# Kernel tuning notes

Hardware: AMD Instinct MI355X
Metric: run time of the kernel (lower is better)

The kernel has to match this reference:

```python
import jax, jax.numpy as jnp
import numpy as np

ALPHA = 4.0  # spikingjelly default Sigmoid surrogate alpha
BN_EPS = 1e-5

@jax.custom_vjp
def _spike(v):
    return (v >= 0.0).astype(v.dtype)

def _spike_fwd(v):
    return _spike(v), v

def _spike_bwd(v, g):
    s = jax.nn.sigmoid(ALPHA * v)
    return (g * ALPHA * s * (1.0 - s),)

_spike.defvjp(_spike_fwd, _spike_bwd)

def lif(x, v_th):
    # Single-step LIFNode(tau=2, v_reset=0) starting from v=0:
    # v = v + (x - v)/tau = x/2 ; spike = Heaviside(v - v_th)
    return _spike(x * 0.5 - v_th)

def bn(x, p):
    # p: [4, C] = gamma, beta, running_mean, running_var (inference BN)
    g, b, m, v = p
    scale = g * jax.lax.rsqrt(v + BN_EPS)
    return x * scale[None, :, None, None] + (b - m * scale)[None, :, None, None]

def conv1x1(x, w):
    # x: [B,C,H,W], w: [O,C]
    return jnp.einsum('bchw,oc->bohw', x, w)

def dwconv3x3(x, w):
    # depthwise 3x3, w: [C,3,3]
    C = x.shape[1]
    return jax.lax.conv_general_dilated(
        x, w[:, None], (1, 1), 'SAME',
        feature_group_count=C,
        dimension_numbers=('NCHW', 'OIHW', 'NCHW'))

def branch(x, w1, dw, w2, bns):
    # RepConv: conv1x1 -> BN -> (dw3x3 -> pw1x1 -> BN), then the extra Sequential BN
    x = bn(conv1x1(x, w1), bns[0])
    x = bn(conv1x1(dwconv3x3(x, dw), w2), bns[1])
    return bn(x, bns[2])

def setup_inputs() -> dict:
    key = jax.random.key(0)
    ks = jax.random.split(key, 5)
    B, C, H, W = 16, 256, 80, 80
    x = jax.random.normal(ks[0], (B, C, H, W), jnp.float32) * 2.0  # so LIFs actually fire
    w1 = jax.random.normal(ks[1], (4, C, C), jnp.float32) * 0.06
    dw = jax.random.normal(ks[2], (4, C, 3, 3), jnp.float32) * 0.3
    w2 = jax.random.normal(ks[3], (4, C, C), jnp.float32) * 0.06
    bn_params = jax.random.uniform(ks[4], (4, 3, 4, C), jnp.float32, 0.1, 1.0)
    return {"x": x, "w1": w1, "dw": dw, "w2": w2, "bn_params": bn_params}

def reference(x, w1, dw, w2, bn_params):
    scale = 0.125
    xs = lif(x, 1.0)                                   # head_lif
    q = branch(xs, w1[0], dw[0], w2[0], bn_params[0])  # q_conv (q_lif unused in source)
    k = branch(xs, w1[1], dw[1], w2[1], bn_params[1])  # k_conv (k_lif unused in source)
    v = branch(xs, w1[2], dw[2], w2[2], bn_params[2])  # v_conv
    v = lif(v, 1.0)                                    # v_lif -> binary spikes
    # k.transpose(-2,-1) @ v : per (b,c) [W,H] @ [H,W] -> [W,W]
    kv = jnp.einsum('bchw,bchu->bcwu', k, v)
    # q @ kv : [H,W] @ [W,W] -> [H,W]
    attn = jnp.einsum('bchw,bcwu->bchu', q, kv) * scale
    s = lif(attn, 0.5)                                 # attn_lif, v_threshold=0.5
    return branch(s, w1[3], dw[3], w2[3], bn_params[3])  # proj_conv
```

## Files before the change

### kernel.cpp

```cpp
#include <hip/hip_runtime.h>
#include <hip/hip_bf16.h>
#include <cstdint>
#include <cstddef>
#include <cmath>

typedef unsigned short u16;
typedef unsigned char  u8;
typedef unsigned int   u32;
typedef __attribute__((ext_vector_type(8))) short short8;
typedef __attribute__((ext_vector_type(4))) float f32x4;
typedef __attribute__((ext_vector_type(4))) u16 u16x4;

#define CCH 256
#define HWP 6400

__device__ __forceinline__ u16 f2bf(float f) {
  u32 u = __float_as_uint(f);
  u = (u + 0x7FFFu + ((u >> 16) & 1u)) >> 16;
  return (u16)u;
}
__device__ __forceinline__ float bf2f(u16 h) { return __uint_as_float(((u32)h) << 16); }
__device__ __forceinline__ void split3(float v, u16& h, u16& m, u16& l) {
  h = f2bf(v); float r = v - bf2f(h);
  m = f2bf(r); l = f2bf(r - bf2f(m));
}
__device__ __forceinline__ void gl_lds16(const void* g, void* l) {
  __builtin_amdgcn_global_load_lds((const __attribute__((address_space(1))) unsigned int*)g,
                                   (__attribute__((address_space(3))) unsigned int*)l,
                                   16, 0, 0);
}

__global__ __launch_bounds__(256) void fold_weights(
    const float* __restrict__ w1, const float* __restrict__ w2,
    const float* __restrict__ bnp,
    u16* __restrict__ w1h, u16* __restrict__ w1m, u16* __restrict__ w1l,
    u16* __restrict__ w2h, u16* __restrict__ w2m, u16* __restrict__ w2l,
    float* __restrict__ b0f, float* __restrict__ b2f)
{
  int i = blockIdx.x >> 8, o = blockIdx.x & 255, c = threadIdx.x;
  const float* bp = bnp + i * 3072;
  double g0 = bp[0 + o],    be0 = bp[256 + o],  m0 = bp[512 + o],  v0 = bp[768 + o];
  double g1 = bp[1024 + o], be1 = bp[1280 + o], m1 = bp[1536 + o], v1 = bp[1792 + o];
  double g2 = bp[2048 + o], be2 = bp[2304 + o], m2 = bp[2560 + o], v2 = bp[2816 + o];
  double s0 = g0 / sqrt(v0 + 1e-5);
  double s1 = g1 / sqrt(v1 + 1e-5);
  double s2 = g2 / sqrt(v2 + 1e-5);
  size_t ro = (size_t)(i * 256 + o) * 256;
  float wa = (float)(s0 * (double)w1[ro + c]);
  float wb = (float)(s1 * s2 * (double)w2[ro + c]);
  u16 h, m, l;
  split3(wa, h, m, l); w1h[ro + c] = h; w1m[ro + c] = m; w1l[ro + c] = l;
  split3(wb, h, m, l); w2h[ro + c] = h; w2m[ro + c] = m; w2l[ro + c] = l;
  if (c == 0) {
    b0f[i * 256 + o] = (float)(be0 - m0 * s0);
    b2f[i * 256 + o] = (float)(s2 * (be1 - m1 * s1) + be2 - m2 * s2);
  }
}

__global__ __launch_bounds__(256) void head_spike(
    const float* __restrict__ x, u8* __restrict__ xs, int b0)
{
  __shared__ u8 tile[64][68];
  int z = blockIdx.z, c0 = blockIdx.y << 6, p0 = blockIdx.x << 6;
  int tid = threadIdx.x;
  const float* xb = x + ((size_t)(b0 + z) * CCH + c0) * HWP + p0;
#pragma unroll
  for (int j = 0; j < 16; ++j) {
    int idx = j * 256 + tid;
    int cl = idx >> 6, pl = idx & 63;
    tile[pl][cl] = (xb[(size_t)cl * HWP + pl] >= 2.0f) ? 1 : 0;
  }
  __syncthreads();
#pragma unroll
  for (int j = 0; j < 4; ++j) {
    int idx = j * 256 + tid;
    int row = idx >> 4, c4 = (idx & 15) << 2;
    *(uchar4*)(xs + ((size_t)z * HWP + p0 + row) * CCH + c0 + c4) =
        *(const uchar4*)&tile[row][c4];
  }
}

__global__ __launch_bounds__(256) void transpose_s(
    const u8* __restrict__ in, u8* __restrict__ out, int b0)
{
  __shared__ u8 tile[64][68];
  int z = blockIdx.z, c0 = blockIdx.y << 6, p0 = blockIdx.x << 6;
  int tid = threadIdx.x;
#pragma unroll
  for (int j = 0; j < 4; ++j) {
    int idx = j * 256 + tid;
    int cl = idx >> 4, p4 = (idx & 15) << 2;
    uchar4 v = *(const uchar4*)(in + ((size_t)z * CCH + c0 + cl) * HWP + p0 + p4);
    tile[p4 + 0][cl] = v.x; tile[p4 + 1][cl] = v.y;
    tile[p4 + 2][cl] = v.z; tile[p4 + 3][cl] = v.w;
  }
  __syncthreads();
#pragma unroll
  for (int j = 0; j < 4; ++j) {
    int idx = j * 256 + tid;
    int row = idx >> 4, c4 = (idx & 15) << 2;
    *(uchar4*)(out + ((size_t)(b0 + z) * HWP + p0 + row) * CCH + c0 + c4) =
        *(const uchar4*)&tile[row][c4];
  }
}

__global__ __launch_bounds__(256) void gemm1(
    const u8* __restrict__ act, int b0in,
    const u16* __restrict__ WH, const u16* __restrict__ WM, const u16* __restrict__ WL,
    const float* __restrict__ bias, float* __restrict__ T1)
{
  __shared__ alignas(16) u16 As[128 * 40];
  const int tid = threadIdx.x, wave = tid >> 6, lane = tid & 63;
  const int p0 = blockIdx.x * 128, o0 = blockIdx.y * 128, z = blockIdx.z;
  const int wm = (wave >> 1) * 64, wn = (wave & 1) * 64;
  const int lc = lane & 15, lr = lane >> 4;
  const u8* ab = act + ((size_t)(b0in + z) * HWP + p0) * CCH;

  f32x4 acc[4][4];
#pragma unroll
  for (int i = 0; i < 4; ++i)
#pragma unroll
    for (int j = 0; j < 4; ++j) acc[i][j] = (f32x4){0.f, 0.f, 0.f, 0.f};

  const int srow = tid >> 1, shalf = tid & 1;

  for (int kc = 0; kc < 8; ++kc) {
    __syncthreads();
    uint4 u = *(const uint4*)(ab + (size_t)srow * CCH + kc * 32 + shalf * 16);
    u32 vv[4] = {u.x, u.y, u.z, u.w};
    u32 w[8];
#pragma unroll
    for (int q = 0; q < 4; ++q) {
      u32 v = vv[q];
      w[2 * q]     = ((v & 255u) ? 0x3F80u : 0u) | (((v >> 8) & 255u) ? 0x3F800000u : 0u);
      w[2 * q + 1] = (((v >> 16) & 255u) ? 0x3F80u : 0u) | (((v >> 24) & 255u) ? 0x3F800000u : 0u);
    }
    *(uint4*)&As[srow * 40 + shalf * 16]     = (uint4){w[0], w[1], w[2], w[3]};
    *(uint4*)&As[srow * 40 + shalf * 16 + 8] = (uint4){w[4], w[5], w[6], w[7]};
    __syncthreads();
    short8 af[4];
#pragma unroll
    for (int i = 0; i < 4; ++i)
      af[i] = *(const short8*)&As[(wm + i * 16 + lc) * 40 + lr * 8];
#pragma unroll
    for (int j = 0; j < 4; ++j) {
      size_t wo = (size_t)(o0 + wn + j * 16 + lc) * CCH + kc * 32 + lr * 8;
      short8 bh = *(const short8*)(WH + wo);
      short8 bm = *(const short8*)(WM + wo);
      short8 bl = *(const short8*)(WL + wo);
#pragma unroll
      for (int i = 0; i < 4; ++i) {
        acc[i][j] = __builtin_amdgcn_mfma_f32_16x16x32_bf16(af[i], bl, acc[i][j], 0, 0, 0);
        acc[i][j] = __builtin_amdgcn_mfma_f32_16x16x32_bf16(af[i], bm, acc[i][j], 0, 0, 0);
        acc[i][j] = __builtin_amdgcn_mfma_f32_16x16x32_bf16(af[i], bh, acc[i][j], 0, 0, 0);
      }
    }
  }
  float* tb = T1 + ((size_t)z * HWP + p0) * CCH + o0;
#pragma unroll
  for (int j = 0; j < 4; ++j) {
    int n = wn + j * 16 + lc;
    float bn_ = bias[o0 + n];
#pragma unroll
    for (int i = 0; i < 4; ++i) {
      int m = wm + i * 16 + lr * 4;
#pragma unroll
      for (int r = 0; r < 4; ++r)
        tb[(size_t)(m + r) * CCH + n] = acc[i][j][r] + bn_;
    }
  }
}

__global__ __launch_bounds__(256) void dw3(
    const float* __restrict__ t1, const float* __restrict__ dwk,
    u16* __restrict__ oh, u16* __restrict__ om, u16* __restrict__ ol)
{
  __shared__ float wl[2304];
  int tid = threadIdx.x;
#pragma unroll
  for (int t = 0; t < 9; ++t) wl[t * 256 + tid] = dwk[t * 256 + tid];
  int c4 = (tid & 63) << 2;
  int pl = tid >> 6;
  int p = blockIdx.x * 4 + pl;
  int z = blockIdx.y;
  int y = p / 80, x = p - y * 80;
  __syncthreads();
  float a0 = 0.f, a1 = 0.f, a2 = 0.f, a3 = 0.f;
  const float* base = t1 + (size_t)z * HWP * CCH;
  const float* wc = &wl[c4 * 9];
#pragma unroll
  for (int dy = -1; dy <= 1; ++dy) {
    int yy = y + dy;
    bool vy = (unsigned)yy < 80u;
#pragma unroll
    for (int dx = -1; dx <= 1; ++dx) {
      int xx = x + dx;
      if (vy && (unsigned)xx < 80u) {
        float4 v = *(const float4*)(base + (size_t)(yy * 80 + xx) * CCH + c4);
        int t = (dy + 1) * 3 + (dx + 1);
        a0 += wc[t]      * v.x;
        a1 += wc[9 + t]  * v.y;
        a2 += wc[18 + t] * v.z;
        a3 += wc[27 + t] * v.w;
      }
    }
  }
  u16 h0, m0, l0, h1, m1, l1, h2, m2, l2, h3, m3, l3;
  split3(a0, h0, m0, l0);
  split3(a1, h1, m1, l1);
  split3(a2, h2, m2, l2);
  split3(a3, h3, m3, l3);
  u16x4 vh, vm, vlo;
  vh.x = h0; vh.y = h1; vh.z = h2; vh.w = h3;
  vm.x = m0; vm.y = m1; vm.z = m2; vm.w = m3;
  vlo.x = l0; vlo.y = l1; vlo.z = l2; vlo.w = l3;
  size_t addr = ((size_t)z * HWP + p) * CCH + c4;
  *(u16x4*)(oh + addr) = vh;
  *(u16x4*)(om + addr) = vm;
  *(u16x4*)(ol + addr) = vlo;
}

template <int MODE>
__global__ __launch_bounds__(256) void gemm2s(
    const u16* __restrict__ AH, const u16* __restrict__ AM, const u16* __restrict__ AL,
    const u16* __restrict__ WH, const u16* __restrict__ WM, const u16* __restrict__ WL,
    const float* __restrict__ bias, int b0,
    float* __restrict__ outF, u8* __restrict__ outB)
{
  __shared__ alignas(16) u16 LAH[4096];
  __shared__ alignas(16) u16 LAM[4096];
  __shared__ alignas(16) u16 LAL[4096];
  __shared__ alignas(16) u16 LWH[4096];
  __shared__ alignas(16) u16 LWM[4096];
  __shared__ alignas(16) u16 LWL[4096];
  const int tid = threadIdx.x, wave = tid >> 6, lane = tid & 63;
  const int p0 = blockIdx.x * 128, o0 = blockIdx.y * 128, z = blockIdx.z;
  const int wm = (wave >> 1) * 64, wn = (wave & 1) * 64;
  const int lc = lane & 15, lr = lane >> 4;
  const char* ahb = (const char*)(AH + ((size_t)z * HWP + p0) * 256);
  const char* amb = (const char*)(AM + ((size_t)z * HWP + p0) * 256);
  const char* alb = (const char*)(AL + ((size_t)z * HWP + p0) * 256);
  const char* whb = (const char*)(WH + (size_t)o0 * 256);
  const char* wmb = (const char*)(WM + (size_t)o0 * 256);
  const char* wlb = (const char*)(WL + (size_t)o0 * 256);

  f32x4 acc[4][4];
#pragma unroll
  for (int i = 0; i < 4; ++i)
#pragma unroll
    for (int j = 0; j < 4; ++j) acc[i][j] = (f32x4){0.f, 0.f, 0.f, 0.f};

  for (int kc = 0; kc < 8; ++kc) {
    const int kof = kc * 64;
#pragma unroll
    for (int t = 0; t < 2; ++t) {
      int li = t * 256 + tid;
      int row = li >> 2, ch = li & 3;
      size_t so = (size_t)row * 512 + kof + ch * 16;
      int base = (t * 256 + wave * 64) * 8;
      gl_lds16(ahb + so, &LAH[base]);
      gl_lds16(amb + so, &LAM[base]);
      gl_lds16(alb + so, &LAL[base]);
      gl_lds16(whb + so, &LWH[base]);
      gl_lds16(wmb + so, &LWM[base]);
      gl_lds16(wlb + so, &LWL[base]);
    }
    __syncthreads();
    short8 afH[4], afM[4], afL[4];
#pragma unroll
    for (int i = 0; i < 4; ++i) {
      int o = (wm + i * 16 + lc) * 32 + lr * 8;
      afH[i] = *(const short8*)&LAH[o];
      afM[i] = *(const short8*)&LAM[o];
      afL[i] = *(const short8*)&LAL[o];
    }
#pragma unroll
    for (int j = 0; j < 4; ++j) {
      int o = (wn + j * 16 + lc) * 32 + lr * 8;
      short8 bh = *(const short8*)&LWH[o];
      short8 bm = *(const short8*)&LWM[o];
      short8 bl = *(const short8*)&LWL[o];
#pragma unroll
      for (int i = 0; i < 4; ++i) {
        acc[i][j] = __builtin_amdgcn_mfma_f32_16x16x32_bf16(afM[i], bm, acc[i][j], 0, 0, 0);
        acc[i][j] = __builtin_amdgcn_mfma_f32_16x16x32_bf16(afL[i], bh, acc[i][j], 0, 0, 0);
        acc[i][j] = __builtin_amdgcn_mfma_f32_16x16x32_bf16(afH[i], bl, acc[i][j], 0, 0, 0);
        acc[i][j] = __builtin_amdgcn_mfma_f32_16x16x32_bf16(afM[i], bh, acc[i][j], 0, 0, 0);
        acc[i][j] = __builtin_amdgcn_mfma_f32_16x16x32_bf16(afH[i], bm, acc[i][j], 0, 0, 0);
        acc[i][j] = __builtin_amdgcn_mfma_f32_16x16x32_bf16(afH[i], bh, acc[i][j], 0, 0, 0);
      }
    }
    __syncthreads();
  }
#pragma unroll
  for (int j = 0; j < 4; ++j) {
    int n = o0 + wn + j * 16 + lc;
    float bn_ = bias[n];
    size_t rowb = ((size_t)(b0 + z) * CCH + n) * HWP + p0;
#pragma unroll
    for (int i = 0; i < 4; ++i) {
      int m = wm + i * 16 + lr * 4;
      if (MODE == 0) {
        float4 o;
        o.x = acc[i][j][0] + bn_; o.y = acc[i][j][1] + bn_;
        o.z = acc[i][j][2] + bn_; o.w = acc[i][j][3] + bn_;
        *(float4*)(outF + rowb + m) = o;
      } else {
        uchar4 o;
        o.x = (acc[i][j][0] + bn_ >= 2.0f) ? 1 : 0;
        o.y = (acc[i][j][1] + bn_ >= 2.0f) ? 1 : 0;
        o.z = (acc[i][j][2] + bn_ >= 2.0f) ? 1 : 0;
        o.w = (acc[i][j][3] + bn_ >= 2.0f) ? 1 : 0;
        *(uchar4*)(outB + rowb + m) = o;
      }
    }
  }
}

__global__ __launch_bounds__(256) void attn_k(
    const float* __restrict__ qf, const float* __restrict__ kf,
    const u8* __restrict__ vv, u8* __restrict__ s)
{
  __shared__ alignas(16) u16 L[30720];
  u32* LW = (u32*)L;
  const int tid = threadIdx.x, wave = tid >> 6, lane = tid & 63;
  const int lc = lane & 15, lr = lane >> 4;
  const size_t off = (size_t)blockIdx.x * HWP;
  u16* KtH = L;          u16* KtM = L + 7680;
  u16* KtL = L + 15360;  u16* Vt  = L + 23040;
#pragma unroll
  for (int t = 0; t < 60; ++t) LW[t * 256 + tid] = 0u;
  __syncthreads();
#pragma unroll
  for (int t = 0; t < 25; ++t) {
    int idx = t * 256 + tid;
    int h = idx / 80, w = idx - h * 80;
    u16 hh, mm, ll; split3(kf[off + idx], hh, mm, ll);
    KtH[w * 96 + h] = hh; KtM[w * 96 + h] = mm; KtL[w * 96 + h] = ll;
    Vt[w * 96 + h] = vv[off + idx] ? (u16)0x3F80 : (u16)0;
  }
  __syncthreads();
  f32x4 kvacc[7];
#pragma unroll
  for (int t = 0; t < 7; ++t) {
    int ti = wave + 4 * t;
    if (ti < 25) {
      int tm = (ti / 5) * 16, tn = (ti % 5) * 16;
      f32x4 a = (f32x4){0.f, 0.f, 0.f, 0.f};
#pragma unroll
      for (int kc = 0; kc < 3; ++kc) {
        int ao = (tm + lc) * 96 + kc * 32 + lr * 8;
        short8 vfr = *(const short8*)&Vt[(tn + lc) * 96 + kc * 32 + lr * 8];
        short8 kl_ = *(const short8*)&KtL[ao];
        short8 km_ = *(const short8*)&KtM[ao];
        short8 kh_ = *(const short8*)&KtH[ao];
        a = __builtin_amdgcn_mfma_f32_16x16x32_bf16(kl_, vfr, a, 0, 0, 0);
        a = __builtin_amdgcn_mfma_f32_16x16x32_bf16(km_, vfr, a, 0, 0, 0);
        a = __builtin_amdgcn_mfma_f32_16x16x32_bf16(kh_, vfr, a, 0, 0, 0);
      }
      kvacc[t] = a;
    }
  }
  __syncthreads();
  u16* QsH = L;          u16* QsM = L + 7680;  u16* QsL = L + 15360;
  u16* KVH = L + 23040;  u16* KVM = L + 24576; u16* KVL = L + 26112;
#pragma unroll
  for (int t = 0; t < 8; ++t) {
    int i = t * 256 + tid;
    if (i < 1920) {
      int arr = i / 640, rem = i - arr * 640;
      LW[arr * 3840 + (rem >> 3) * 48 + 40 + (rem & 7)] = 0u;
    }
  }
  if (tid < 384) {
    int arr = tid >> 7, rem = tid & 127;
    LW[11520 + arr * 768 + (rem >> 3) * 48 + 40 + (rem & 7)] = 0u;
  }
#pragma unroll
  for (int t = 0; t < 25; ++t) {
    int idx = t * 256 + tid;
    int h = idx / 80, w = idx - h * 80;
    u16 hh, mm, ll; split3(qf[off + idx], hh, mm, ll);
    QsH[h * 96 + w] = hh; QsM[h * 96 + w] = mm; QsL[h * 96 + w] = ll;
  }
  for (int ut = 0; ut < 5; ++ut) {
    __syncthreads();
#pragma unroll
    for (int t = 0; t < 7; ++t) {
      int ti = wave + 4 * t;
      if (ti < 25 && (ti % 5) == ut) {
        int tm = (ti / 5) * 16;
#pragma unroll
        for (int r = 0; r < 4; ++r) {
          u16 hh, mm, ll; split3(kvacc[t][r], hh, mm, ll);
          int o = lc * 96 + tm + lr * 4 + r;
          KVH[o] = hh; KVM[o] = mm; KVL[o] = ll;
        }
      }
    }
    __syncthreads();
    for (int th = wave; th < 5; th += 4) {
      int hm = th * 16;
      f32x4 a = (f32x4){0.f, 0.f, 0.f, 0.f};
#pragma unroll
      for (int kc = 0; kc < 3; ++kc) {
        int qo = (hm + lc) * 96 + kc * 32 + lr * 8;
        int ko = lc * 96 + kc * 32 + lr * 8;
        short8 qh_ = *(const short8*)&QsH[qo];
        short8 qm_ = *(const short8*)&QsM[qo];
        short8 ql_ = *(const short8*)&QsL[qo];
        short8 kh_ = *(const short8*)&KVH[ko];
        short8 km_ = *(const short8*)&KVM[ko];
        short8 kl_ = *(const short8*)&KVL[ko];
        a = __builtin_amdgcn_mfma_f32_16x16x32_bf16(qm_, km_, a, 0, 0, 0);
        a = __builtin_amdgcn_mfma_f32_16x16x32_bf16(ql_, kh_, a, 0, 0, 0);
        a = __builtin_amdgcn_mfma_f32_16x16x32_bf16(qh_, kl_, a, 0, 0, 0);
        a = __builtin_amdgcn_mfma_f32_16x16x32_bf16(qm_, kh_, a, 0, 0, 0);
        a = __builtin_amdgcn_mfma_f32_16x16x32_bf16(qh_, km_, a, 0, 0, 0);
        a = __builtin_amdgcn_mfma_f32_16x16x32_bf16(qh_, kh_, a, 0, 0, 0);
      }
#pragma unroll
      for (int r = 0; r < 4; ++r)
        s[off + (size_t)(hm + lr * 4 + r) * 80 + ut * 16 + lc] = (a[r] >= 8.0f) ? 1 : 0;
    }
  }
}

extern "C" void kernel_launch(void* const* d_in, const int* in_sizes, int n_in,
                              void* d_out, int out_size, void* d_ws, size_t ws_size,
                              hipStream_t stream)
{
  const float* x   = (const float*)d_in[0];
  const float* w1  = (const float*)d_in[1];
  const float* dwk = (const float*)d_in[2];
  const float* w2  = (const float*)d_in[3];
  const float* bnp = (const float*)d_in[4];
  float* out = (float*)d_out;
  char* ws = (char*)d_ws;

  u16* W1H = (u16*)(ws + 0);
  u16* W1M = (u16*)(ws + 524288);
  u16* W1L = (u16*)(ws + 1048576);
  u16* W2H = (u16*)(ws + 1572864);
  u16* W2M = (u16*)(ws + 2097152);
  u16* W2L = (u16*)(ws + 2621440);
  float* B0F = (float*)(ws + 3145728);
  float* B2F = (float*)(ws + 3149824);
  u8*    SPM = (u8*)(ws + 3153920);
  u8*    XS  = (u8*)(ws + 29368320);
  float* T1  = (float*)(ws + 42475520);
  float* QF  = (float*)(ws + 94904320);
  float* KF  = (float*)(ws + 147333120);
  u8*    V   = (u8*)(ws + 199761920);
  u16*   D2H = (u16*)(ws + 212869120);
  u16*   D2M = (u16*)(ws + 239083520);
  u16*   D2L = (u16*)(ws + 265297920);

  dim3 gb(256);
  fold_weights<<<dim3(1024), gb, 0, stream>>>(w1, w2, bnp,
      W1H, W1M, W1L, W2H, W2M, W2L, B0F, B2F);

  for (int c = 0; c < 2; ++c) {
    int b0 = c * 8;
    dim3 gh(100, 4, 8), gg(50, 2, 8), gd(1600, 8);
    head_spike<<<gh, gb, 0, stream>>>(x, XS, b0);
    gemm1<<<gg, gb, 0, stream>>>(XS, 0, W1H + 0 * 65536, W1M + 0 * 65536, W1L + 0 * 65536,
                                 B0F + 0, T1);
    dw3<<<gd, gb, 0, stream>>>(T1, dwk + 0 * 2304, D2H, D2M, D2L);
    gemm2s<0><<<gg, gb, 0, stream>>>(D2H, D2M, D2L,
                                     W2H + 0 * 65536, W2M + 0 * 65536, W2L + 0 * 65536,
                                     B2F + 0, 0, QF, nullptr);
    gemm1<<<gg, gb, 0, stream>>>(XS, 0, W1H + 1 * 65536, W1M + 1 * 65536, W1L + 1 * 65536,
                                 B0F + 256, T1);
    dw3<<<gd, gb, 0, stream>>>(T1, dwk + 1 * 2304, D2H, D2M, D2L);
    gemm2s<0><<<gg, gb, 0, stream>>>(D2H, D2M, D2L,
                                     W2H + 1 * 65536, W2M + 1 * 65536, W2L + 1 * 65536,
                                     B2F + 256, 0, KF, nullptr);
    gemm1<<<gg, gb, 0, stream>>>(XS, 0, W1H + 2 * 65536, W1M + 2 * 65536, W1L + 2 * 65536,
                                 B0F + 512, T1);
    dw3<<<gd, gb, 0, stream>>>(T1, dwk + 2 * 2304, D2H, D2M, D2L);
    gemm2s<1><<<gg, gb, 0, stream>>>(D2H, D2M, D2L,
                                     W2H + 2 * 65536, W2M + 2 * 65536, W2L + 2 * 65536,
                                     B2F + 512, 0, nullptr, V);
    attn_k<<<dim3(2048), gb, 0, stream>>>(QF, KF, V, V);
    transpose_s<<<gh, gb, 0, stream>>>(V, SPM, b0);
  }
  for (int c = 0; c < 2; ++c) {
    int b0 = c * 8;
    dim3 gg(50, 2, 8), gd(1600, 8);
    gemm1<<<gg, gb, 0, stream>>>(SPM, b0, W1H + 3 * 65536, W1M + 3 * 65536, W1L + 3 * 65536,
                                 B0F + 768, T1);
    dw3<<<gd, gb, 0, stream>>>(T1, dwk + 3 * 2304, D2H, D2M, D2L);
    gemm2s<0><<<gg, gb, 0, stream>>>(D2H, D2M, D2L,
                                     W2H + 3 * 65536, W2M + 3 * 65536, W2L + 3 * 65536,
                                     B2F + 768, b0, out, nullptr);
  }
}
```

Before: 1.632 ms.

## Reassociate attention as (Q·Kᵀ)·V, stage gemm1 weights in LDS, swizzle LDS tiles

The attention kernel now computes (Q Kᵀ) V instead of Q (Kᵀ V). Each of five waves owns a 16-row strip, reads Q straight from global memory, keeps V as bytes in LDS and expands it to bf16 on the fly, and drops the five-iteration per-column synchronised loop. gemm1 now stages weight tiles into LDS with async global-to-LDS copies instead of loading them from global per wave. Both GEMMs use an XOR-like chunk swizzle to avoid LDS bank conflicts. Reassociating changes the floating-point summation order ahead of a hard threshold, so results could shift slightly near the cutoff.

```diff
diff --git a/kernel.cpp b/kernel.cpp
--- a/kernel.cpp
+++ b/kernel.cpp
@@ -110,11 +110,17 @@
     const float* __restrict__ bias, float* __restrict__ T1)
 {
   __shared__ alignas(16) u16 As[128 * 40];
+  __shared__ alignas(16) u16 LWH[4096];
+  __shared__ alignas(16) u16 LWM[4096];
+  __shared__ alignas(16) u16 LWL[4096];
   const int tid = threadIdx.x, wave = tid >> 6, lane = tid & 63;
   const int p0 = blockIdx.x * 128, o0 = blockIdx.y * 128, z = blockIdx.z;
   const int wm = (wave >> 1) * 64, wn = (wave & 1) * 64;
   const int lc = lane & 15, lr = lane >> 4;
   const u8* ab = act + ((size_t)(b0in + z) * HWP + p0) * CCH;
+  const char* whb = (const char*)(WH + (size_t)o0 * 256);
+  const char* wmb = (const char*)(WM + (size_t)o0 * 256);
+  const char* wlb = (const char*)(WL + (size_t)o0 * 256);
 
   f32x4 acc[4][4];
 #pragma unroll
@@ -125,7 +131,19 @@
   const int srow = tid >> 1, shalf = tid & 1;
 
   for (int kc = 0; kc < 8; ++kc) {
+    const int kof = kc * 64;
     __syncthreads();
+#pragma unroll
+    for (int t = 0; t < 2; ++t) {
+      int li = t * 256 + tid;
+      int row = li >> 2, ch = li & 3;
+      int chp = (ch - row - (row >> 2)) & 3;
+      size_t so = (size_t)row * 512 + kof + chp * 16;
+      int base = (t * 256 + wave * 64) * 8;
+      gl_lds16(whb + so, &LWH[base]);
+      gl_lds16(wmb + so, &LWM[base]);
+      gl_lds16(wlb + so, &LWL[base]);
+    }
     uint4 u = *(const uint4*)(ab + (size_t)srow * CCH + kc * 32 + shalf * 16);
     u32 vv[4] = {u.x, u.y, u.z, u.w};
     u32 w[8];
@@ -144,10 +162,11 @@
       af[i] = *(const short8*)&As[(wm + i * 16 + lc) * 40 + lr * 8];
 #pragma unroll
     for (int j = 0; j < 4; ++j) {
-      size_t wo = (size_t)(o0 + wn + j * 16 + lc) * CCH + kc * 32 + lr * 8;
-      short8 bh = *(const short8*)(WH + wo);
-      short8 bm = *(const short8*)(WM + wo);
-      short8 bl = *(const short8*)(WL + wo);
+      int row = wn + j * 16 + lc;
+      int o = row * 32 + ((lr + lc + (lc >> 2)) & 3) * 8;
+      short8 bh = *(const short8*)&LWH[o];
+      short8 bm = *(const short8*)&LWM[o];
+      short8 bl = *(const short8*)&LWL[o];
 #pragma unroll
       for (int i = 0; i < 4; ++i) {
         acc[i][j] = __builtin_amdgcn_mfma_f32_16x16x32_bf16(af[i], bl, acc[i][j], 0, 0, 0);
@@ -256,7 +275,8 @@
     for (int t = 0; t < 2; ++t) {
       int li = t * 256 + tid;
       int row = li >> 2, ch = li & 3;
-      size_t so = (size_t)row * 512 + kof + ch * 16;
+      int chp = (ch - row - (row >> 2)) & 3;
+      size_t so = (size_t)row * 512 + kof + chp * 16;
       int base = (t * 256 + wave * 64) * 8;
       gl_lds16(ahb + so, &LAH[base]);
       gl_lds16(amb + so, &LAM[base]);
@@ -269,14 +289,16 @@
     short8 afH[4], afM[4], afL[4];
 #pragma unroll
     for (int i = 0; i < 4; ++i) {
-      int o = (wm + i * 16 + lc) * 32 + lr * 8;
+      int row = wm + i * 16 + lc;
+      int o = row * 32 + ((lr + lc + (lc >> 2)) & 3) * 8;
       afH[i] = *(const short8*)&LAH[o];
       afM[i] = *(const short8*)&LAM[o];
       afL[i] = *(const short8*)&LAL[o];
     }
 #pragma unroll
     for (int j = 0; j < 4; ++j) {
-      int o = (wn + j * 16 + lc) * 32 + lr * 8;
+      int row = wn + j * 16 + lc;
+      int o = row * 32 + ((lr + lc + (lc >> 2)) & 3) * 8;
       short8 bh = *(const short8*)&LWH[o];
       short8 bm = *(const short8*)&LWM[o];
       short8 bl = *(const short8*)&LWL[o];
@@ -317,113 +339,119 @@
   }
 }
 
-__global__ __launch_bounds__(256) void attn_k(
+__global__ __launch_bounds__(320) void attn_k(
     const float* __restrict__ qf, const float* __restrict__ kf,
     const u8* __restrict__ vv, u8* __restrict__ s)
 {
-  __shared__ alignas(16) u16 L[30720];
-  u32* LW = (u32*)L;
+  __shared__ alignas(16) u16 L[24960];
+  __shared__ alignas(16) u8  VT[8320];
   const int tid = threadIdx.x, wave = tid >> 6, lane = tid & 63;
   const int lc = lane & 15, lr = lane >> 4;
   const size_t off = (size_t)blockIdx.x * HWP;
-  u16* KtH = L;          u16* KtM = L + 7680;
-  u16* KtL = L + 15360;  u16* Vt  = L + 23040;
-#pragma unroll
-  for (int t = 0; t < 60; ++t) LW[t * 256 + tid] = 0u;
-  __syncthreads();
-#pragma unroll
-  for (int t = 0; t < 25; ++t) {
-    int idx = t * 256 + tid;
+  u16* KH = L; u16* KM = L + 8320; u16* KL = L + 16640;
+
+  for (int t = 0; t < 12; ++t) {
+    int i = t * 320 + tid;
+    if (i < 3840) {
+      int pl = i / 1280, rem = i - pl * 1280;
+      L[pl * 8320 + (rem >> 4) * 104 + 80 + (rem & 15)] = 0;
+    }
+  }
+  for (int t = 0; t < 4; ++t) {
+    int i = t * 320 + tid;
+    if (i < 1280) VT[(i >> 4) * 104 + 80 + (i & 15)] = 0;
+  }
+  for (int t = 0; t < 20; ++t) {
+    int idx = t * 320 + tid;
     int h = idx / 80, w = idx - h * 80;
     u16 hh, mm, ll; split3(kf[off + idx], hh, mm, ll);
-    KtH[w * 96 + h] = hh; KtM[w * 96 + h] = mm; KtL[w * 96 + h] = ll;
-    Vt[w * 96 + h] = vv[off + idx] ? (u16)0x3F80 : (u16)0;
+    KH[h * 104 + w] = hh; KM[h * 104 + w] = mm; KL[h * 104 + w] = ll;
+    VT[w * 104 + h] = vv[off + idx];
   }
   __syncthreads();
-  f32x4 kvacc[7];
-#pragma unroll
-  for (int t = 0; t < 7; ++t) {
-    int ti = wave + 4 * t;
-    if (ti < 25) {
-      int tm = (ti / 5) * 16, tn = (ti % 5) * 16;
-      f32x4 a = (f32x4){0.f, 0.f, 0.f, 0.f};
-#pragma unroll
-      for (int kc = 0; kc < 3; ++kc) {
-        int ao = (tm + lc) * 96 + kc * 32 + lr * 8;
-        short8 vfr = *(const short8*)&Vt[(tn + lc) * 96 + kc * 32 + lr * 8];
-        short8 kl_ = *(const short8*)&KtL[ao];
-        short8 km_ = *(const short8*)&KtM[ao];
-        short8 kh_ = *(const short8*)&KtH[ao];
-        a = __builtin_amdgcn_mfma_f32_16x16x32_bf16(kl_, vfr, a, 0, 0, 0);
-        a = __builtin_amdgcn_mfma_f32_16x16x32_bf16(km_, vfr, a, 0, 0, 0);
-        a = __builtin_amdgcn_mfma_f32_16x16x32_bf16(kh_, vfr, a, 0, 0, 0);
+
+  f32x4 accS[5];
+#pragma unroll
+  for (int n = 0; n < 5; ++n) accS[n] = (f32x4){0.f, 0.f, 0.f, 0.f};
+  const int hrow = wave * 16 + lc;
+  for (int kc = 0; kc < 3; ++kc) {
+    short8 qh, qm, ql;
+    int w0 = kc * 32 + lr * 8;
+    if (w0 < 80) {
+      const float* qp = qf + off + hrow * 80 + w0;
+      float4 a = *(const float4*)qp;
+      float4 b = *(const float4*)(qp + 4);
+      float qv[8] = {a.x, a.y, a.z, a.w, b.x, b.y, b.z, b.w};
+#pragma unroll
+      for (int e = 0; e < 8; ++e) {
+        u16 hh, mm, ll; split3(qv[e], hh, mm, ll);
+        qh[e] = (short)hh; qm[e] = (short)mm; ql[e] = (short)ll;
       }
-      kvacc[t] = a;
+    } else {
+      qh = (short8){0,0,0,0,0,0,0,0}; qm = qh; ql = qh;
+    }
+#pragma unroll
+    for (int n = 0; n < 5; ++n) {
+      int bo = (n * 16 + lc) * 104 + kc * 32 + lr * 8;
+      short8 kh_ = *(const short8*)&KH[bo];
+      short8 km_ = *(const short8*)&KM[bo];
+      short8 kl_ = *(const short8*)&KL[bo];
+      accS[n] = __builtin_amdgcn_mfma_f32_16x16x32_bf16(qh, kl_, accS[n], 0, 0, 0);
+      accS[n] = __builtin_amdgcn_mfma_f32_16x16x32_bf16(ql, kh_, accS[n], 0, 0, 0);
+      accS[n] = __builtin_amdgcn_mfma_f32_16x16x32_bf16(qm, km_, accS[n], 0, 0, 0);
+      accS[n] = __builtin_amdgcn_mfma_f32_16x16x32_bf16(qm, kh_, accS[n], 0, 0, 0);
+      accS[n] = __builtin_amdgcn_mfma_f32_16x16x32_bf16(qh, km_, accS[n], 0, 0, 0);
+      accS[n] = __builtin_amdgcn_mfma_f32_16x16x32_bf16(qh, kh_, accS[n], 0, 0, 0);
     }
   }
   __syncthreads();
-  u16* QsH = L;          u16* QsM = L + 7680;  u16* QsL = L + 15360;
-  u16* KVH = L + 23040;  u16* KVM = L + 24576; u16* KVL = L + 26112;
-#pragma unroll
-  for (int t = 0; t < 8; ++t) {
-    int i = t * 256 + tid;
-    if (i < 1920) {
-      int arr = i / 640, rem = i - arr * 640;
-      LW[arr * 3840 + (rem >> 3) * 48 + 40 + (rem & 7)] = 0u;
-    }
-  }
-  if (tid < 384) {
-    int arr = tid >> 7, rem = tid & 127;
-    LW[11520 + arr * 768 + (rem >> 3) * 48 + 40 + (rem & 7)] = 0u;
-  }
-#pragma unroll
-  for (int t = 0; t < 25; ++t) {
-    int idx = t * 256 + tid;
-    int h = idx / 80, w = idx - h * 80;
-    u16 hh, mm, ll; split3(qf[off + idx], hh, mm, ll);
-    QsH[h * 96 + w] = hh; QsM[h * 96 + w] = mm; QsL[h * 96 + w] = ll;
-  }
-  for (int ut = 0; ut < 5; ++ut) {
-    __syncthreads();
-#pragma unroll
-    for (int t = 0; t < 7; ++t) {
-      int ti = wave + 4 * t;
-      if (ti < 25 && (ti % 5) == ut) {
-        int tm = (ti / 5) * 16;
-#pragma unroll
-        for (int r = 0; r < 4; ++r) {
-          u16 hh, mm, ll; split3(kvacc[t][r], hh, mm, ll);
-          int o = lc * 96 + tm + lr * 4 + r;
-          KVH[o] = hh; KVM[o] = mm; KVL[o] = ll;
-        }
-      }
-    }
-    __syncthreads();
-    for (int th = wave; th < 5; th += 4) {
-      int hm = th * 16;
-      f32x4 a = (f32x4){0.f, 0.f, 0.f, 0.f};
-#pragma unroll
-      for (int kc = 0; kc < 3; ++kc) {
-        int qo = (hm + lc) * 96 + kc * 32 + lr * 8;
-        int ko = lc * 96 + kc * 32 + lr * 8;
-        short8 qh_ = *(const short8*)&QsH[qo];
-        short8 qm_ = *(const short8*)&QsM[qo];
-        short8 ql_ = *(const short8*)&QsL[qo];
-        short8 kh_ = *(const short8*)&KVH[ko];
-        short8 km_ = *(const short8*)&KVM[ko];
-        short8 kl_ = *(const short8*)&KVL[ko];
-        a = __builtin_amdgcn_mfma_f32_16x16x32_bf16(qm_, km_, a, 0, 0, 0);
-        a = __builtin_amdgcn_mfma_f32_16x16x32_bf16(ql_, kh_, a, 0, 0, 0);
-        a = __builtin_amdgcn_mfma_f32_16x16x32_bf16(qh_, kl_, a, 0, 0, 0);
-        a = __builtin_amdgcn_mfma_f32_16x16x32_bf16(qm_, kh_, a, 0, 0, 0);
-        a = __builtin_amdgcn_mfma_f32_16x16x32_bf16(qh_, km_, a, 0, 0, 0);
-        a = __builtin_amdgcn_mfma_f32_16x16x32_bf16(qh_, kh_, a, 0, 0, 0);
-      }
-#pragma unroll
-      for (int r = 0; r < 4; ++r)
-        s[off + (size_t)(hm + lr * 4 + r) * 80 + ut * 16 + lc] = (a[r] >= 8.0f) ? 1 : 0;
-    }
-  }
+  for (int t = 0; t < 12; ++t) {
+    int i = t * 320 + tid;
+    if (i < 3840) {
+      int pl = i / 1280, rem = i - pl * 1280;
+      L[pl * 8320 + (rem >> 4) * 104 + 80 + (rem & 15)] = 0;
+    }
+  }
+#pragma unroll
+  for (int n = 0; n < 5; ++n) {
+#pragma unroll
+    for (int r = 0; r < 4; ++r) {
+      u16 hh, mm, ll; split3(accS[n][r], hh, mm, ll);
+      int o = (wave * 16 + lr * 4 + r) * 104 + n * 16 + lc;
+      KH[o] = hh; KM[o] = mm; KL[o] = ll;
+    }
+  }
+  __syncthreads();
+  f32x4 accA[5];
+#pragma unroll
+  for (int n = 0; n < 5; ++n) accA[n] = (f32x4){0.f, 0.f, 0.f, 0.f};
+  for (int kc = 0; kc < 3; ++kc) {
+    int ao = (wave * 16 + lc) * 104 + kc * 32 + lr * 8;
+    short8 sh_ = *(const short8*)&KH[ao];
+    short8 sm_ = *(const short8*)&KM[ao];
+    short8 sl_ = *(const short8*)&KL[ao];
+#pragma unroll
+    for (int n = 0; n < 5; ++n) {
+      const u8* vp = &VT[(n * 16 + lc) * 104 + kc * 32 + lr * 8];
+      u32 b0 = *(const u32*)vp;
+      u32 b1 = *(const u32*)(vp + 4);
+      u32 e0 = ((b0 & 255u) ? 0x3F80u : 0u) | (((b0 >> 8) & 255u) ? 0x3F800000u : 0u);
+      u32 e1 = (((b0 >> 16) & 255u) ? 0x3F80u : 0u) | (((b0 >> 24) & 255u) ? 0x3F800000u : 0u);
+      u32 e2 = ((b1 & 255u) ? 0x3F80u : 0u) | (((b1 >> 8) & 255u) ? 0x3F800000u : 0u);
+      u32 e3 = (((b1 >> 16) & 255u) ? 0x3F80u : 0u) | (((b1 >> 24) & 255u) ? 0x3F800000u : 0u);
+      u32 vbw[4] = {e0, e1, e2, e3};
+      short8 vb = *(const short8*)vbw;
+      accA[n] = __builtin_amdgcn_mfma_f32_16x16x32_bf16(sl_, vb, accA[n], 0, 0, 0);
+      accA[n] = __builtin_amdgcn_mfma_f32_16x16x32_bf16(sm_, vb, accA[n], 0, 0, 0);
+      accA[n] = __builtin_amdgcn_mfma_f32_16x16x32_bf16(sh_, vb, accA[n], 0, 0, 0);
+    }
+  }
+#pragma unroll
+  for (int n = 0; n < 5; ++n)
+#pragma unroll
+    for (int r = 0; r < 4; ++r)
+      s[off + (size_t)(wave * 16 + lr * 4 + r) * 80 + n * 16 + lc] =
+          (accA[n][r] >= 8.0f) ? 1 : 0;
 }
 
 extern "C" void kernel_launch(void* const* d_in, const int* in_sizes, int n_in,
@@ -482,7 +510,7 @@
     gemm2s<1><<<gg, gb, 0, stream>>>(D2H, D2M, D2L,
                                      W2H + 2 * 65536, W2M + 2 * 65536, W2L + 2 * 65536,
                                      B2F + 512, 0, nullptr, V);
-    attn_k<<<dim3(2048), gb, 0, stream>>>(QF, KF, V, V);
+    attn_k<<<dim3(2048), dim3(320), 0, stream>>>(QF, KF, V, V);
     transpose_s<<<gh, gb, 0, stream>>>(V, SPM, b0);
   }
   for (int c = 0; c < 2; ++c) {
```

After: 1.398 ms. 14.3% less time.
